# Kernel optimization log

Hardware: AMD Instinct MI355X
Metric: run time of the kernel (lower is better)

Reference implementation:

```python
import jax, jax.numpy as jnp
import numpy as np

NUM_HEADS = 16
BUDGET = 1024


def layer_norm(x, g, b, eps=1e-5):
    mu = jnp.mean(x, axis=-1, keepdims=True)
    var = jnp.mean((x - mu) ** 2, axis=-1, keepdims=True)
    return (x - mu) / jnp.sqrt(var + eps) * g + b


def setup_inputs() -> dict:
    key = jax.random.key(0)
    ks = jax.random.split(key, 6)
    B, N, D = 2, 2048, 1024
    H, Dh = NUM_HEADS, 1024 // NUM_HEADS
    sc = 1.0 / np.sqrt(D).astype(np.float32)
    X = jax.random.normal(ks[0], (B, N, D), jnp.float32)
    W_q = jax.random.normal(ks[1], (D, D), jnp.float32) * sc
    W_k = jax.random.normal(ks[2], (D, D), jnp.float32) * sc
    W_v = jax.random.normal(ks[3], (D, D), jnp.float32) * sc
    W_o = jax.random.normal(ks[4], (D, D), jnp.float32) * sc
    return dict(
        X=X, W_q=W_q, W_k=W_k, W_v=W_v, W_o=W_o,
        gamma_q=jnp.ones((D,), jnp.float32), beta_q=jnp.zeros((D,), jnp.float32),
        gamma_k=jnp.ones((D,), jnp.float32), beta_k=jnp.zeros((D,), jnp.float32),
        cache_k=jnp.zeros((B, H, BUDGET, Dh), jnp.float32),
        cache_v=jnp.zeros((B, H, BUDGET, Dh), jnp.float32),
        start_pos=0,
    )


def reference(X, W_q, W_k, W_v, W_o, gamma_q, beta_q, gamma_k, beta_k,
              cache_k, cache_v, start_pos):
    B, N, D = X.shape
    H = NUM_HEADS
    Dh = D // H
    budget = cache_k.shape[2]
    M = start_pos + N  # total kv length

    XQ = layer_norm(X @ W_q, gamma_q, beta_q).reshape(B, N, H, Dh).transpose(0, 2, 1, 3)
    XK = layer_norm(X @ W_k, gamma_k, beta_k).reshape(B, N, H, Dh).transpose(0, 2, 1, 3)
    XV = (X @ W_v).reshape(B, N, H, Dh).transpose(0, 2, 1, 3)

    K = jnp.concatenate([cache_k[:B, :, :start_pos], XK], axis=2)  # (B,H,M,Dh)
    V = jnp.concatenate([cache_v[:B, :, :start_pos], XV], axis=2)

    logits = jnp.einsum('bhnd,bhmd->bhnm', XQ, K) / np.float32(np.sqrt(Dh))
    n_idx = jnp.arange(N)[:, None]
    m_idx = jnp.arange(M)[None, :]
    causal_keep = (m_idx < start_pos) | ((m_idx - start_pos) <= n_idx)  # (N,M)
    logits = jnp.where(causal_keep, logits, -jnp.inf)

    # --- selection (eviction) scores from head 0 ---
    S = jax.nn.relu(logits[:, 0])                        # (B,N,M); relu(-inf)=0
    S = S.at[:, :, start_pos].set(0.0)                   # never evict <BOS>-like slot
    S = S.at[:, :, start_pos:].multiply(1.0 - jnp.eye(N, dtype=S.dtype))  # zero diagonal
    S = jnp.roll(S, 1, axis=1).at[:, 0, :].set(0.0)      # shift: scores apply from next query
    Fm = jnp.cumsum(S, axis=1)                           # (B,N,M) cumulative eviction scores

    # --- sequential heavy-hitter eviction ---
    unmasked0 = jnp.broadcast_to(jnp.arange(budget, dtype=jnp.int32), (B, budget))
    kpos = jnp.arange(budget, dtype=jnp.int32)[None, :]

    def step(unmasked, i):
        new_idx = jnp.concatenate(
            [unmasked, jnp.full((B, 1), i, unmasked.dtype)], axis=1)     # (B,budget+1)
        row = jax.lax.dynamic_index_in_dim(Fm, i - start_pos, axis=1, keepdims=False)  # (B,M)
        scores = jnp.take_along_axis(row, new_idx, axis=1)
        idx = jnp.argmax(scores, axis=-1)                                # (B,)
        evicted = jnp.take_along_axis(new_idx, idx[:, None], axis=1)[:, 0]
        unmasked = jnp.where(kpos < idx[:, None], new_idx[:, :budget], new_idx[:, 1:])
        return unmasked, evicted

    steps = jnp.arange(max(budget, start_pos), M, dtype=jnp.int32)       # (T,)
    _, evicts = jax.lax.scan(step, unmasked0, steps)                     # evicts (T,B)

    big = jnp.int32(M + start_pos + 1)
    evict_time = jnp.full((B, M), big, jnp.int32)
    evict_time = evict_time.at[jnp.arange(B, dtype=jnp.int32)[None, :], evicts].min(steps[:, None])
    # query row j is pruned from key m iff (j + start_pos) >= evict_time[m]
    prune_keep = (jnp.arange(N)[:, None] + start_pos) < evict_time[:, None, :]  # (B,N,M)

    logits = jnp.where(prune_keep[:, None], logits, -jnp.inf)
    attn = jax.nn.softmax(logits, axis=-1)
    O = jnp.einsum('bhnm,bhmd->bhnd', attn, V).transpose(0, 2, 1, 3).reshape(B, N, D)
    return O @ W_o
```

## Files before the change

### kernel.cpp

```cpp
#include <hip/hip_runtime.h>

#define B_    2
#define N_    2048
#define D_    1024
#define H_    16
#define DH_   64
#define M_    2048
#define ROWS_ 4096
#define BUD_  1024

typedef unsigned short u16;
typedef unsigned int   u32;
typedef unsigned long long u64;
typedef __attribute__((ext_vector_type(8))) short short8;
typedef __attribute__((ext_vector_type(4))) float floatx4;

__device__ __forceinline__ u16 f2b(float f) {
    u32 u = __float_as_uint(f);
    return (u16)((u + 0x7FFFu + ((u >> 16) & 1u)) >> 16);
}
__device__ __forceinline__ float b2f(u16 h) {
    return __uint_as_float(((u32)h) << 16);
}

__global__ __launch_bounds__(256) void cast_x_kernel(
    const float* __restrict__ X, u16* __restrict__ Xhi, u16* __restrict__ Xlo)
{
    int idx = (blockIdx.x * 256 + threadIdx.x) * 4;
    float4 v = *(const float4*)&X[idx];
    u16 h0 = f2b(v.x), h1 = f2b(v.y), h2 = f2b(v.z), h3 = f2b(v.w);
    ushort4 hv; hv.x = h0; hv.y = h1; hv.z = h2; hv.w = h3;
    *(ushort4*)&Xhi[idx] = hv;
    ushort4 lv;
    lv.x = f2b(v.x - b2f(h0)); lv.y = f2b(v.y - b2f(h1));
    lv.z = f2b(v.z - b2f(h2)); lv.w = f2b(v.w - b2f(h3));
    *(ushort4*)&Xlo[idx] = lv;
}

__global__ __launch_bounds__(1024) void cast_w_kernel(
    const float* __restrict__ W, u16* __restrict__ Whi, u16* __restrict__ Wlo,
    int do_lo)
{
    __shared__ float tile[32][33];
    int tx = threadIdx.x, ty = threadIdx.y;
    int x = blockIdx.x * 32 + tx, y = blockIdx.y * 32 + ty;
    tile[ty][tx] = W[(size_t)y * D_ + x];
    __syncthreads();
    float v = tile[tx][ty];
    int n = blockIdx.x * 32 + ty, k = blockIdx.y * 32 + tx;
    u16 h = f2b(v);
    Whi[(size_t)n * D_ + k] = h;
    if (do_lo) Wlo[(size_t)n * D_ + k] = f2b(v - b2f(h));
}

template<int MODE>
__device__ void gemm_core(
    const u16* __restrict__ Ah, const u16* __restrict__ Al,
    const u16* __restrict__ Bh, const u16* __restrict__ Bl,
    float* __restrict__ C, int bx, int m0)
{
    __shared__ __align__(16) u16 sAh[128 * 32];
    __shared__ __align__(16) u16 sBh[128 * 32];
    __shared__ __align__(16) u16 sAl[MODE ? 128 * 32 : 8];
    __shared__ __align__(16) u16 sBl[MODE ? 128 * 32 : 8];
    int tid = threadIdx.x;
    int lane = tid & 63, wv = tid >> 6;
    int wr = wv >> 1, wc = wv & 1;
    int quad = lane >> 4, l16 = lane & 15;
    int n0 = bx * 128;

    floatx4 acc[4][4];
    floatx4 zero = {0.f, 0.f, 0.f, 0.f};
#pragma unroll
    for (int i = 0; i < 4; ++i)
#pragma unroll
        for (int j = 0; j < 4; ++j) acc[i][j] = zero;

    for (int k0 = 0; k0 < 1024; k0 += 32) {
#pragma unroll
        for (int it = 0; it < 2; ++it) {
            int e = (tid + it * 256) * 8;
            int r = e >> 5, c = e & 31;
            *(uint4*)&sAh[e] = *(const uint4*)&Ah[(size_t)(m0 + r) * 1024 + k0 + c];
            *(uint4*)&sBh[e] = *(const uint4*)&Bh[(size_t)(n0 + r) * 1024 + k0 + c];
            if (MODE) {
                *(uint4*)&sAl[e] = *(const uint4*)&Al[(size_t)(m0 + r) * 1024 + k0 + c];
                *(uint4*)&sBl[e] = *(const uint4*)&Bl[(size_t)(n0 + r) * 1024 + k0 + c];
            }
        }
        __syncthreads();
        short8 ah[4], al[4], bh[4], bl[4];
#pragma unroll
        for (int x = 0; x < 4; ++x) {
            int ra = (wr * 64 + x * 16 + l16) * 32 + quad * 8;
            int rb = (wc * 64 + x * 16 + l16) * 32 + quad * 8;
            ah[x] = *(const short8*)&sAh[ra];
            bh[x] = *(const short8*)&sBh[rb];
            if (MODE) {
                al[x] = *(const short8*)&sAl[ra];
                bl[x] = *(const short8*)&sBl[rb];
            }
        }
#pragma unroll
        for (int mi = 0; mi < 4; ++mi)
#pragma unroll
            for (int ni = 0; ni < 4; ++ni) {
                acc[mi][ni] = __builtin_amdgcn_mfma_f32_16x16x32_bf16(
                    ah[mi], bh[ni], acc[mi][ni], 0, 0, 0);
                if (MODE) {
                    acc[mi][ni] = __builtin_amdgcn_mfma_f32_16x16x32_bf16(
                        ah[mi], bl[ni], acc[mi][ni], 0, 0, 0);
                    acc[mi][ni] = __builtin_amdgcn_mfma_f32_16x16x32_bf16(
                        al[mi], bh[ni], acc[mi][ni], 0, 0, 0);
                }
            }
        __syncthreads();
    }
#pragma unroll
    for (int mi = 0; mi < 4; ++mi)
#pragma unroll
        for (int ni = 0; ni < 4; ++ni)
#pragma unroll
            for (int r = 0; r < 4; ++r) {
                int row = m0 + wr * 64 + mi * 16 + quad * 4 + r;
                int col = n0 + wc * 64 + ni * 16 + l16;
                C[(size_t)row * 1024 + col] = acc[mi][ni][r];
            }
}

__global__ __launch_bounds__(256) void gemm_qkv_kernel(
    const u16* __restrict__ Xhi, const u16* __restrict__ Xlo,
    const u16* __restrict__ Wqh, const u16* __restrict__ Wql,
    const u16* __restrict__ Wkh, const u16* __restrict__ Wkl,
    const u16* __restrict__ Wvh,
    float* __restrict__ Yq, float* __restrict__ Yk, float* __restrict__ Yv)
{
    int m0 = blockIdx.y * 128;
    if (blockIdx.z == 0)
        gemm_core<1>(Xhi, Xlo, Wqh, Wql, Yq, blockIdx.x, m0);
    else if (blockIdx.z == 1)
        gemm_core<1>(Xhi, Xlo, Wkh, Wkl, Yk, blockIdx.x, m0);
    else
        gemm_core<0>(Xhi, nullptr, Wvh, nullptr, Yv, blockIdx.x, m0);
}

template<int MODE>
__global__ __launch_bounds__(256) void gemm_kernel_t(
    const u16* __restrict__ Ah, const u16* __restrict__ Al,
    const u16* __restrict__ Bh, const u16* __restrict__ Bl,
    float* __restrict__ C, int ymode)
{
    int by = blockIdx.y;
    int yidx = (ymode == 0) ? by : ((by < 8) ? by + 8 : by + 16);
    gemm_core<MODE>(Ah, Al, Bh, Bl, C, blockIdx.x, yidx * 128);
}

__global__ __launch_bounds__(256) void lnpack_all_kernel(
    const float* __restrict__ Yq, const float* __restrict__ Yk,
    const float* __restrict__ Yv,
    const float* __restrict__ gq, const float* __restrict__ bq,
    const float* __restrict__ gk, const float* __restrict__ bk,
    u16* __restrict__ Qb, u16* __restrict__ Kb, u16* __restrict__ Vb,
    float* __restrict__ q0s, float* __restrict__ k0s)
{
    const float* Y; const float* gamma; const float* beta;
    u16* Pk; float* head0; int do_ln;
    if (blockIdx.y == 0) { Y = Yq; gamma = gq; beta = bq; Pk = Qb; head0 = q0s; do_ln = 1; }
    else if (blockIdx.y == 1) { Y = Yk; gamma = gk; beta = bk; Pk = Kb; head0 = k0s; do_ln = 1; }
    else { Y = Yv; gamma = nullptr; beta = nullptr; Pk = Vb; head0 = nullptr; do_ln = 0; }

    int r = blockIdx.x;
    int tid = threadIdx.x;
    float4 v = *(const float4*)&Y[(size_t)r * D_ + tid * 4];
    float mu = 0.f, rsig = 1.f;
    __shared__ float sS[4], sQ[4];
    if (do_ln) {
        float s = v.x + v.y + v.z + v.w;
        float q = v.x * v.x + v.y * v.y + v.z * v.z + v.w * v.w;
#pragma unroll
        for (int d = 1; d < 64; d <<= 1) { s += __shfl_xor(s, d); q += __shfl_xor(q, d); }
        if ((tid & 63) == 0) { sS[tid >> 6] = s; sQ[tid >> 6] = q; }
        __syncthreads();
        s = sS[0] + sS[1] + sS[2] + sS[3];
        q = sQ[0] + sQ[1] + sQ[2] + sQ[3];
        mu = s * (1.f / 1024.f);
        float var = q * (1.f / 1024.f) - mu * mu;
        rsig = rsqrtf(var + 1e-5f);
    }
    int b = r >> 11, n = r & 2047;
    float xs[4] = {v.x, v.y, v.z, v.w};
#pragma unroll
    for (int j = 0; j < 4; ++j) {
        int c = tid * 4 + j;
        float val = do_ln ? ((xs[j] - mu) * rsig * gamma[c] + beta[c]) : xs[j];
        int h = c >> 6, dh = c & 63;
        Pk[(((size_t)b * H_ + h) * N_ + n) * DH_ + dh] = f2b(val);
        if (head0 && c < 64) head0[(size_t)r * 64 + c] = val;
    }
}

__global__ __launch_bounds__(256) void s64_kernel(
    const float* __restrict__ q0, const float* __restrict__ k0,
    float* __restrict__ S)
{
    int b = blockIdx.z;
    int n0 = blockIdx.y * 64, m0 = blockIdx.x * 64;
    int tid = threadIdx.x;
    int tx = tid & 15, ty = tid >> 4;
    floatx4 zero = {0.f, 0.f, 0.f, 0.f};
    if (m0 > n0 + 63) {
#pragma unroll
        for (int i = 0; i < 4; ++i) {
            int n = n0 + 4 * ty + i;
            *(floatx4*)&S[((size_t)b * N_ + n) * M_ + m0 + 4 * tx] = zero;
        }
        return;
    }
    __shared__ float sq[64][65], sk[64][65];
    {
        int r = tid >> 2, cseg = (tid & 3) * 16;
        const float* qrow = &q0[((size_t)b * N_ + n0 + r) * 64 + cseg];
        const float* krow = &k0[((size_t)b * N_ + m0 + r) * 64 + cseg];
#pragma unroll
        for (int u = 0; u < 4; ++u) {
            float4 qa = *(const float4*)&qrow[u * 4];
            sq[r][cseg + u * 4 + 0] = qa.x; sq[r][cseg + u * 4 + 1] = qa.y;
            sq[r][cseg + u * 4 + 2] = qa.z; sq[r][cseg + u * 4 + 3] = qa.w;
            float4 ka = *(const float4*)&krow[u * 4];
            sk[r][cseg + u * 4 + 0] = ka.x; sk[r][cseg + u * 4 + 1] = ka.y;
            sk[r][cseg + u * 4 + 2] = ka.z; sk[r][cseg + u * 4 + 3] = ka.w;
        }
    }
    __syncthreads();
    float acc[4][4];
#pragma unroll
    for (int i = 0; i < 4; ++i)
#pragma unroll
        for (int j = 0; j < 4; ++j) acc[i][j] = 0.f;
#pragma unroll 8
    for (int d = 0; d < 64; ++d) {
        float qv[4], kv[4];
#pragma unroll
        for (int i = 0; i < 4; ++i) qv[i] = sq[4 * ty + i][d];
#pragma unroll
        for (int j = 0; j < 4; ++j) kv[j] = sk[4 * tx + j][d];
#pragma unroll
        for (int i = 0; i < 4; ++i)
#pragma unroll
            for (int j = 0; j < 4; ++j) acc[i][j] += qv[i] * kv[j];
    }
#pragma unroll
    for (int i = 0; i < 4; ++i) {
        int n = n0 + 4 * ty + i;
        floatx4 out;
#pragma unroll
        for (int j = 0; j < 4; ++j) {
            int m = m0 + 4 * tx + j;
            out[j] = (m < n && m != 0) ? fmaxf(acc[i][j] * 0.125f, 0.f) : 0.f;
        }
        *(floatx4*)&S[((size_t)b * N_ + n) * M_ + m0 + 4 * tx] = out;
    }
}

__global__ __launch_bounds__(256) void p_kernel(const float* __restrict__ S,
                                                float* __restrict__ P)
{
    int b = blockIdx.z, c = blockIdx.y;
    int m = blockIdx.x * 256 + threadIdx.x;
    const float* base = S + ((size_t)b * N_ + c * 128) * M_ + m;
    float s = 0.f;
    for (int j = 0; j < 128; ++j) s += base[(size_t)j * M_];
    P[((size_t)b * 8 + c) * M_ + m] = s;
}

__device__ __forceinline__ void vsel(float& va, u32& la, float vb, u32 lb) {
    bool tk = vb > va;
    va = tk ? vb : va;
    la = tk ? lb : la;
}

template<int CTRL, int RMASK>
__device__ __forceinline__ void dpp_max_pack(float& v, u32& lo) {
    int hi = __float_as_int(v);
    int hi_o = __builtin_amdgcn_update_dpp(hi, hi, CTRL, RMASK, 0xF, false);
    int lo_o = __builtin_amdgcn_update_dpp((int)lo, (int)lo, CTRL, RMASK, 0xF, false);
    long long a = (long long)((((u64)(u32)hi) << 32) | lo);
    long long b = (long long)((((u64)(u32)hi_o) << 32) | (u32)lo_o);
    bool tk = b > a;
    v = tk ? __int_as_float(hi_o) : v;
    lo = tk ? (u32)lo_o : lo;
}

__device__ __forceinline__ void wave_argmax_to63(float& v, u32& lo) {
    dpp_max_pack<0x121, 0xF>(v, lo);
    dpp_max_pack<0x122, 0xF>(v, lo);
    dpp_max_pack<0x124, 0xF>(v, lo);
    dpp_max_pack<0x128, 0xF>(v, lo);
    dpp_max_pack<0x142, 0xA>(v, lo);
    dpp_max_pack<0x143, 0xC>(v, lo);
}

#define GLOAD(dst, voff, ptr, imm)                                    \
    asm volatile("global_load_dwordx4 %0, %1, %2 offset:" #imm        \
                 : "=v"(dst) : "v"(voff), "s"(ptr) : "memory")

#define ISSUE2(bank, row)                                             \
    {                                                                 \
        u32 r_ = (u32)((row) < 2047 ? (row) : 2047);                  \
        u32 vo = wbyte + r_ * 8192u;                                  \
        GLOAD(bank[0], vo, Sb, 0);                                    \
        GLOAD(bank[1], vo, Sb, 1024);                                 \
    }

#define VWAIT6()                                                      \
    do { asm volatile("s_waitcnt vmcnt(6)" ::: "memory");             \
         __builtin_amdgcn_sched_barrier(0); } while (0)
#define VWAIT0()                                                      \
    do { asm volatile("s_waitcnt vmcnt(0)" ::: "memory");             \
         __builtin_amdgcn_sched_barrier(0); } while (0)

__device__ __forceinline__ void evict_step4(
    int i, int t, int w, int par,
    const u32 (&lov)[2][4], float (&cum)[2][4], int (&evti)[2][4],
    const floatx4 (&bank)[2], uint2 (*spair)[4])
{
    const float NEGINF = __uint_as_float(0xFF800000u);
    float v0 = cum[0][0]; u32 l0 = lov[0][0];
    vsel(v0, l0, cum[0][1], lov[0][1]);
    float v1 = cum[0][2]; u32 l1 = lov[0][2];
    vsel(v1, l1, cum[0][3], lov[0][3]);
    vsel(v0, l0, v1, l1);
    float v2 = cum[1][0]; u32 l2 = lov[1][0];
    vsel(v2, l2, cum[1][1], lov[1][1]);
    float v3 = cum[1][2]; u32 l3 = lov[1][2];
    vsel(v3, l3, cum[1][3], lov[1][3]);
    vsel(v2, l2, v3, l3);
    vsel(v0, l0, v2, l2);
    wave_argmax_to63(v0, l0);
    if (t == 63) spair[par][w] = make_uint2(l0, (u32)__float_as_int(v0));
    asm volatile("s_waitcnt lgkmcnt(0)" ::: "memory");
    __builtin_amdgcn_sched_barrier(0);
    __builtin_amdgcn_s_barrier();
    __builtin_amdgcn_sched_barrier(0);
    uint2 q0 = spair[par][0], q1 = spair[par][1];
    uint2 q2 = spair[par][2], q3 = spair[par][3];
    long long k0 = (long long)((((u64)q0.y) << 32) | q0.x);
    long long k1 = (long long)((((u64)q1.y) << 32) | q1.x);
    long long k2 = (long long)((((u64)q2.y) << 32) | q2.x);
    long long k3 = (long long)((((u64)q3.y) << 32) | q3.x);
    long long ba = k0 > k1 ? k0 : k1;
    long long bb = k2 > k3 ? k2 : k3;
    long long bst = ba > bb ? ba : bb;
    const u32 lostar = (u32)(bst & 0xFFFFFFFFll);
#pragma unroll
    for (int c = 0; c < 2; ++c) {
        cum[c][0] += bank[c][0]; cum[c][1] += bank[c][1];
        cum[c][2] += bank[c][2]; cum[c][3] += bank[c][3];
    }
#pragma unroll
    for (int c = 0; c < 2; ++c)
#pragma unroll
        for (int e = 0; e < 4; ++e) {
            bool hit = (lov[c][e] == lostar);
            cum[c][e] = hit ? NEGINF : cum[c][e];
            evti[c][e] = hit ? i : evti[c][e];
        }
}

__device__ void evict_role(const float* __restrict__ S,
                           const float* __restrict__ P,
                           int* __restrict__ evt)
{
    int b = blockIdx.x;
    int tid = threadIdx.x;
    int w = tid >> 6, t = tid & 63;
    const float* Sb = S + (size_t)b * N_ * M_;
    int* evtb = evt + b * M_;
    const int mbase = 512 * w + 4 * t;
    const u32 wbyte = (u32)(2048 * w + 16 * t);
    __shared__ uint2 spair[2][4];
    u32 lov[2][4];
    int evti[2][4];
#pragma unroll
    for (int c = 0; c < 2; ++c)
#pragma unroll
        for (int e = 0; e < 4; ++e) {
            lov[c][e] = (u32)(2048 - (mbase + 256 * c + e));
            evti[c][e] = 0x3FFFFFFF;
        }
    float cum[2][4];
#pragma unroll
    for (int c = 0; c < 2; ++c) {
        float ax = 0.f, ay = 0.f, az = 0.f, aw = 0.f;
#pragma unroll
        for (int cc = 0; cc < 8; ++cc) {
            floatx4 pv = *(const floatx4*)&P[((size_t)b * 8 + cc) * M_ + mbase + 256 * c];
            ax += pv[0]; ay += pv[1]; az += pv[2]; aw += pv[3];
        }
        cum[c][0] = ax; cum[c][1] = ay; cum[c][2] = az; cum[c][3] = aw;
    }
    VWAIT0();
    floatx4 bA[2], bB[2], bC[2], bD[2];
    ISSUE2(bA, 1024)
    ISSUE2(bB, 1025)
    ISSUE2(bC, 1026)
    ISSUE2(bD, 1027)
#pragma unroll 1
    for (int ip = 1024; ip < 2048; ip += 4) {
        VWAIT6();
        evict_step4(ip + 0, t, w, 0, lov, cum, evti, bA, spair);
        ISSUE2(bA, ip + 4)
        VWAIT6();
        evict_step4(ip + 1, t, w, 1, lov, cum, evti, bB, spair);
        ISSUE2(bB, ip + 5)
        VWAIT6();
        evict_step4(ip + 2, t, w, 0, lov, cum, evti, bC, spair);
        ISSUE2(bC, ip + 6)
        VWAIT6();
        evict_step4(ip + 3, t, w, 1, lov, cum, evti, bD, spair);
        ISSUE2(bD, ip + 7)
    }
    VWAIT0();
#pragma unroll
    for (int c = 0; c < 2; ++c) {
        int4 o; o.x = evti[c][0]; o.y = evti[c][1];
        o.z = evti[c][2]; o.w = evti[c][3];
        *(int4*)&evtb[mbase + 256 * c] = o;
    }
}

__device__ void flash_role(
    const u16* __restrict__ Qb, const u16* __restrict__ Kb,
    const u16* __restrict__ Vb, const int* __restrict__ evtg,
    u16* __restrict__ Ob, int bh, int q0, int ktiles)
{
    int b = bh >> 4, h = bh & 15;
    int tid = threadIdx.x, lane = tid & 63, w = tid >> 6;
    int quad = lane >> 4, l16 = lane & 15;
    const u16* Qh = Qb + (size_t)bh * N_ * DH_;
    const u16* Kh = Kb + (size_t)bh * N_ * DH_;
    const u16* Vh = Vb + (size_t)bh * N_ * DH_;
    __shared__ __align__(16) u16 sK[64 * 64];
    __shared__ __align__(16) u16 sV[64 * 64];
    __shared__ __align__(16) u16 sP[4][16 * 64];
    __shared__ int sevt[64];

    short8 aq0 = *(const short8*)&Qh[(size_t)(q0 + w * 16 + l16) * 64 + quad * 8];
    short8 aq1 = *(const short8*)&Qh[(size_t)(q0 + w * 16 + l16) * 64 + quad * 8 + 32];

    floatx4 zero = {0.f, 0.f, 0.f, 0.f};
    floatx4 accO[4];
#pragma unroll
    for (int d = 0; d < 4; ++d) accO[d] = zero;
    float m_i[4] = {-1e30f, -1e30f, -1e30f, -1e30f};
    float l_i[4] = {0.f, 0.f, 0.f, 0.f};

    for (int kt = 0; kt < ktiles; ++kt) {
        int k0 = kt * 64;
#pragma unroll
        for (int it = 0; it < 2; ++it) {
            int e = (tid + it * 256) * 8;
            int r = e >> 6, c = e & 63;
            *(uint4*)&sK[e] = *(const uint4*)&Kh[(size_t)(k0 + r) * 64 + c];
            uint4 vv = *(const uint4*)&Vh[(size_t)(k0 + r) * 64 + c];
            sV[(c + 0) * 64 + r] = (u16)(vv.x & 0xFFFF);
            sV[(c + 1) * 64 + r] = (u16)(vv.x >> 16);
            sV[(c + 2) * 64 + r] = (u16)(vv.y & 0xFFFF);
            sV[(c + 3) * 64 + r] = (u16)(vv.y >> 16);
            sV[(c + 4) * 64 + r] = (u16)(vv.z & 0xFFFF);
            sV[(c + 5) * 64 + r] = (u16)(vv.z >> 16);
            sV[(c + 6) * 64 + r] = (u16)(vv.w & 0xFFFF);
            sV[(c + 7) * 64 + r] = (u16)(vv.w >> 16);
        }
        if (evtg && tid < 64) sevt[tid] = evtg[b * M_ + k0 + tid];
        __syncthreads();

        floatx4 lg[4];
        int nbase = q0 + w * 16 + quad * 4;
#pragma unroll
        for (int s = 0; s < 4; ++s) {
            floatx4 sc = zero;
            short8 bk0 = *(const short8*)&sK[(s * 16 + l16) * 64 + quad * 8];
            short8 bk1 = *(const short8*)&sK[(s * 16 + l16) * 64 + quad * 8 + 32];
            sc = __builtin_amdgcn_mfma_f32_16x16x32_bf16(aq0, bk0, sc, 0, 0, 0);
            sc = __builtin_amdgcn_mfma_f32_16x16x32_bf16(aq1, bk1, sc, 0, 0, 0);
            int m = k0 + s * 16 + l16;
            int ev = evtg ? sevt[s * 16 + l16] : 0x7FFFFFFF;
#pragma unroll
            for (int r = 0; r < 4; ++r) {
                int n = nbase + r;
                bool keep = (m <= n) && (n < ev);
                lg[s][r] = keep ? sc[r] * 0.125f : -1e30f;
            }
        }
        float mnew[4], scale[4], rs[4];
#pragma unroll
        for (int r = 0; r < 4; ++r) {
            float mx = fmaxf(fmaxf(lg[0][r], lg[1][r]), fmaxf(lg[2][r], lg[3][r]));
#pragma unroll
            for (int d = 1; d < 16; d <<= 1) mx = fmaxf(mx, __shfl_xor(mx, d));
            mnew[r] = fmaxf(m_i[r], mx);
            scale[r] = __expf(m_i[r] - mnew[r]);
            m_i[r] = mnew[r];
            rs[r] = 0.f;
        }
#pragma unroll
        for (int s = 0; s < 4; ++s)
#pragma unroll
            for (int r = 0; r < 4; ++r) {
                float p = __expf(lg[s][r] - mnew[r]);
                rs[r] += p;
                sP[w][(quad * 4 + r) * 64 + s * 16 + l16] = f2b(p);
            }
#pragma unroll
        for (int r = 0; r < 4; ++r) {
            float t_ = rs[r];
#pragma unroll
            for (int d = 1; d < 16; d <<= 1) t_ += __shfl_xor(t_, d);
            l_i[r] = l_i[r] * scale[r] + t_;
        }
#pragma unroll
        for (int dd = 0; dd < 4; ++dd) {
            accO[dd][0] *= scale[0]; accO[dd][1] *= scale[1];
            accO[dd][2] *= scale[2]; accO[dd][3] *= scale[3];
        }
        short8 ap0 = *(const short8*)&sP[w][l16 * 64 + quad * 8];
        short8 ap1 = *(const short8*)&sP[w][l16 * 64 + quad * 8 + 32];
#pragma unroll
        for (int dd = 0; dd < 4; ++dd) {
            short8 bv0 = *(const short8*)&sV[(dd * 16 + l16) * 64 + quad * 8];
            short8 bv1 = *(const short8*)&sV[(dd * 16 + l16) * 64 + quad * 8 + 32];
            accO[dd] = __builtin_amdgcn_mfma_f32_16x16x32_bf16(ap0, bv0, accO[dd], 0, 0, 0);
            accO[dd] = __builtin_amdgcn_mfma_f32_16x16x32_bf16(ap1, bv1, accO[dd], 0, 0, 0);
        }
        __syncthreads();
    }
#pragma unroll
    for (int dd = 0; dd < 4; ++dd)
#pragma unroll
        for (int r = 0; r < 4; ++r) {
            int n = q0 + w * 16 + quad * 4 + r;
            int col = h * 64 + dd * 16 + l16;
            Ob[((size_t)b * N_ + n) * D_ + col] = f2b(accO[dd][r] / l_i[r]);
        }
}

__global__ __launch_bounds__(256) void fused_evict_flash1(
    const float* __restrict__ S, const float* __restrict__ P,
    int* __restrict__ evt,
    const u16* __restrict__ Qb, const u16* __restrict__ Kb,
    const u16* __restrict__ Vb, u16* __restrict__ Ob)
{
    if (blockIdx.x < 2) {
        evict_role(S, P, evt);
    } else {
        int fid = blockIdx.x - 2;
        int bh = fid >> 4, j = fid & 15;
        flash_role(Qb, Kb, Vb, nullptr, Ob, bh, j * 64, j + 1);
    }
}

__global__ __launch_bounds__(256) void fused_flash2_gemmo1(
    const u16* __restrict__ Qb, const u16* __restrict__ Kb,
    const u16* __restrict__ Vb, const int* __restrict__ evt,
    u16* __restrict__ Ob, const u16* __restrict__ Woh,
    float* __restrict__ Out)
{
    if (blockIdx.x < 512) {
        int fid = blockIdx.x;
        int bh = fid >> 4, j = (fid & 15) + 16;
        flash_role(Qb, Kb, Vb, evt, Ob, bh, j * 64, j + 1);
    } else {
        int gid = blockIdx.x - 512;
        int bx = gid & 7, gy = gid >> 3;
        int yidx = (gy < 8) ? gy : gy + 8;
        gemm_core<0>((const u16*)Ob, nullptr, Woh, nullptr, Out, bx, yidx * 128);
    }
}

extern "C" void kernel_launch(void* const* d_in, const int* in_sizes, int n_in,
                              void* d_out, int out_size, void* d_ws, size_t ws_size,
                              hipStream_t stream)
{
    (void)in_sizes; (void)n_in; (void)out_size; (void)ws_size;
    const float* X  = (const float*)d_in[0];
    const float* Wq = (const float*)d_in[1];
    const float* Wk = (const float*)d_in[2];
    const float* Wv = (const float*)d_in[3];
    const float* Wo = (const float*)d_in[4];
    const float* gq = (const float*)d_in[5];
    const float* bq = (const float*)d_in[6];
    const float* gk = (const float*)d_in[7];
    const float* bk = (const float*)d_in[8];

    char* p = (char*)d_ws;
    const size_t SZ_XH = (size_t)ROWS_ * D_ * 2;
    const size_t SZ_W  = (size_t)D_ * D_ * 2;
    const size_t SZ_Y  = (size_t)ROWS_ * D_ * 4;
    const size_t SZ_PK = (size_t)ROWS_ * D_ * 2;
    const size_t SZ_H0 = (size_t)ROWS_ * 64 * 4;

    size_t o = 0;
    u16* Xhi = (u16*)(p + o); o += SZ_XH;
    u16* Xlo = (u16*)(p + o); o += SZ_XH;
    u16* Wqh = (u16*)(p + o); o += SZ_W;
    u16* Wql = (u16*)(p + o); o += SZ_W;
    u16* Wkh = (u16*)(p + o); o += SZ_W;
    u16* Wkl = (u16*)(p + o); o += SZ_W;
    u16* Wvh = (u16*)(p + o); o += SZ_W;
    u16* Woh = (u16*)(p + o); o += SZ_W;
    float* Yq = (float*)(p + o); size_t oYq = o; o += SZ_Y;
    float* Yk = (float*)(p + o); o += SZ_Y;
    float* Yv = (float*)(p + o); o += SZ_Y;
    u16* Qb = (u16*)(p + o); o += SZ_PK;
    u16* Kb = (u16*)(p + o); o += SZ_PK;
    u16* Vb = (u16*)(p + o); o += SZ_PK;
    float* q0s = (float*)(p + o); o += SZ_H0;
    float* k0s = (float*)(p + o); o += SZ_H0;
    float* Pp  = (float*)(p + o); o += (size_t)B_ * 8 * M_ * 4;
    int* evt   = (int*)(p + o);  o += (size_t)B_ * M_ * 4;
    float* S = (float*)(p + oYq);
    u16* Ob  = Xhi;

    cast_x_kernel<<<ROWS_ * D_ / (256 * 4), 256, 0, stream>>>(X, Xhi, Xlo);
    dim3 wgrid(32, 32), wblk(32, 32);
    cast_w_kernel<<<wgrid, wblk, 0, stream>>>(Wq, Wqh, Wql, 1);
    cast_w_kernel<<<wgrid, wblk, 0, stream>>>(Wk, Wkh, Wkl, 1);
    cast_w_kernel<<<wgrid, wblk, 0, stream>>>(Wv, Wvh, nullptr, 0);
    cast_w_kernel<<<wgrid, wblk, 0, stream>>>(Wo, Woh, nullptr, 0);

    gemm_qkv_kernel<<<dim3(8, 32, 3), 256, 0, stream>>>(
        Xhi, Xlo, Wqh, Wql, Wkh, Wkl, Wvh, Yq, Yk, Yv);

    lnpack_all_kernel<<<dim3(ROWS_, 3), 256, 0, stream>>>(
        Yq, Yk, Yv, gq, bq, gk, bk, Qb, Kb, Vb, q0s, k0s);

    s64_kernel<<<dim3(M_ / 64, N_ / 64, B_), 256, 0, stream>>>(q0s, k0s, S);
    p_kernel<<<dim3(M_ / 256, 8, B_), 256, 0, stream>>>(S, Pp);

    fused_evict_flash1<<<514, 256, 0, stream>>>(S, Pp, evt, Qb, Kb, Vb, Ob);
    fused_flash2_gemmo1<<<640, 256, 0, stream>>>(
        Qb, Kb, Vb, evt, Ob, Woh, (float*)d_out);
    gemm_kernel_t<0><<<dim3(8, 16), 256, 0, stream>>>(
        (const u16*)Ob, nullptr, Woh, nullptr, (float*)d_out, 2);
}
```

Baseline: 766.0 us.

## Resolve two serial eviction steps per block barrier using top-2 reduction

The serial eviction scan now handles two time steps per workgroup barrier. Step i's argmax is computed as before. For step i+1, each wave computes a best and second-best candidate with a DPP top-2 reduction over the updated cumulative scores, and after the barrier the second winner is taken as the best candidate other than the first winner. This halves the number of s_barrier and LDS round trips in the 1024-step serial loop, at the cost of more VALU work per step (64-bit packed compares and a top-2 reduction) and a changed load-wait depth.

```diff
diff --git a/kernel.cpp b/kernel.cpp
--- a/kernel.cpp
+++ b/kernel.cpp
@@ -273,31 +273,40 @@
     P[((size_t)b * 8 + c) * M_ + m] = s;
 }
 
-__device__ __forceinline__ void vsel(float& va, u32& la, float vb, u32 lb) {
-    bool tk = vb > va;
-    va = tk ? vb : va;
-    la = tk ? lb : la;
-}
-
+__device__ __forceinline__ long long maxll(long long a, long long b) {
+    return a > b ? a : b;
+}
+__device__ __forceinline__ long long mkpack(float v, u32 lo) {
+    return (long long)((((u64)(u32)__float_as_int(v)) << 32) | (u64)lo);
+}
 template<int CTRL, int RMASK>
-__device__ __forceinline__ void dpp_max_pack(float& v, u32& lo) {
-    int hi = __float_as_int(v);
-    int hi_o = __builtin_amdgcn_update_dpp(hi, hi, CTRL, RMASK, 0xF, false);
-    int lo_o = __builtin_amdgcn_update_dpp((int)lo, (int)lo, CTRL, RMASK, 0xF, false);
-    long long a = (long long)((((u64)(u32)hi) << 32) | lo);
-    long long b = (long long)((((u64)(u32)hi_o) << 32) | (u32)lo_o);
-    bool tk = b > a;
-    v = tk ? __int_as_float(hi_o) : v;
-    lo = tk ? (u32)lo_o : lo;
-}
-
-__device__ __forceinline__ void wave_argmax_to63(float& v, u32& lo) {
-    dpp_max_pack<0x121, 0xF>(v, lo);
-    dpp_max_pack<0x122, 0xF>(v, lo);
-    dpp_max_pack<0x124, 0xF>(v, lo);
-    dpp_max_pack<0x128, 0xF>(v, lo);
-    dpp_max_pack<0x142, 0xA>(v, lo);
-    dpp_max_pack<0x143, 0xC>(v, lo);
+__device__ __forceinline__ long long dpp_ll(long long p) {
+    int hi = (int)((u64)p >> 32), lo = (int)(u32)(u64)p;
+    int ho = __builtin_amdgcn_update_dpp(hi, hi, CTRL, RMASK, 0xF, false);
+    int lo2 = __builtin_amdgcn_update_dpp(lo, lo, CTRL, RMASK, 0xF, false);
+    return (long long)((((u64)(u32)ho) << 32) | (u32)lo2);
+}
+template<int CTRL, int RMASK>
+__device__ __forceinline__ void dpp_t1(long long& B) {
+    B = maxll(B, dpp_ll<CTRL, RMASK>(B));
+}
+template<int CTRL, int RMASK>
+__device__ __forceinline__ void dpp_t2(long long& B, long long& S) {
+    long long Bo = dpp_ll<CTRL, RMASK>(B);
+    long long So = dpp_ll<CTRL, RMASK>(S);
+    bool gt = Bo > B;
+    long long nS = gt ? maxll(B, So) : maxll(S, Bo);
+    B = gt ? Bo : B;
+    S = nS;
+}
+__device__ __forceinline__ long long wave_t1_63(long long B) {
+    dpp_t1<0x121, 0xF>(B); dpp_t1<0x122, 0xF>(B); dpp_t1<0x124, 0xF>(B);
+    dpp_t1<0x128, 0xF>(B); dpp_t1<0x142, 0xA>(B); dpp_t1<0x143, 0xC>(B);
+    return B;
+}
+__device__ __forceinline__ void wave_t2_63(long long& B, long long& S) {
+    dpp_t2<0x121, 0xF>(B, S); dpp_t2<0x122, 0xF>(B, S); dpp_t2<0x124, 0xF>(B, S);
+    dpp_t2<0x128, 0xF>(B, S); dpp_t2<0x142, 0xA>(B, S); dpp_t2<0x143, 0xC>(B, S);
 }
 
 #define GLOAD(dst, voff, ptr, imm)                                    \
@@ -312,59 +321,86 @@
         GLOAD(bank[1], vo, Sb, 1024);                                 \
     }
 
-#define VWAIT6()                                                      \
-    do { asm volatile("s_waitcnt vmcnt(6)" ::: "memory");             \
+#define VWAIT4()                                                      \
+    do { asm volatile("s_waitcnt vmcnt(4)" ::: "memory");             \
          __builtin_amdgcn_sched_barrier(0); } while (0)
 #define VWAIT0()                                                      \
     do { asm volatile("s_waitcnt vmcnt(0)" ::: "memory");             \
          __builtin_amdgcn_sched_barrier(0); } while (0)
 
-__device__ __forceinline__ void evict_step4(
+__device__ __forceinline__ long long pk2(uint2 q) {
+    return (long long)((((u64)q.y) << 32) | q.x);
+}
+
+__device__ __forceinline__ void evict_pair(
     int i, int t, int w, int par,
     const u32 (&lov)[2][4], float (&cum)[2][4], int (&evti)[2][4],
-    const floatx4 (&bank)[2], uint2 (*spair)[4])
+    const floatx4 (&bi)[2], const floatx4 (&bi1)[2],
+    uint2 (*spair)[4][3])
 {
     const float NEGINF = __uint_as_float(0xFF800000u);
-    float v0 = cum[0][0]; u32 l0 = lov[0][0];
-    vsel(v0, l0, cum[0][1], lov[0][1]);
-    float v1 = cum[0][2]; u32 l1 = lov[0][2];
-    vsel(v1, l1, cum[0][3], lov[0][3]);
-    vsel(v0, l0, v1, l1);
-    float v2 = cum[1][0]; u32 l2 = lov[1][0];
-    vsel(v2, l2, cum[1][1], lov[1][1]);
-    float v3 = cum[1][2]; u32 l3 = lov[1][2];
-    vsel(v3, l3, cum[1][3], lov[1][3]);
-    vsel(v2, l2, v3, l3);
-    vsel(v0, l0, v2, l2);
-    wave_argmax_to63(v0, l0);
-    if (t == 63) spair[par][w] = make_uint2(l0, (u32)__float_as_int(v0));
+    long long a = mkpack(cum[0][0], lov[0][0]);
+    a = maxll(a, mkpack(cum[0][1], lov[0][1]));
+    a = maxll(a, mkpack(cum[0][2], lov[0][2]));
+    a = maxll(a, mkpack(cum[0][3], lov[0][3]));
+    a = maxll(a, mkpack(cum[1][0], lov[1][0]));
+    a = maxll(a, mkpack(cum[1][1], lov[1][1]));
+    a = maxll(a, mkpack(cum[1][2], lov[1][2]));
+    a = maxll(a, mkpack(cum[1][3], lov[1][3]));
+    a = wave_t1_63(a);
+#pragma unroll
+    for (int c = 0; c < 2; ++c) {
+        cum[c][0] += bi[c][0]; cum[c][1] += bi[c][1];
+        cum[c][2] += bi[c][2]; cum[c][3] += bi[c][3];
+    }
+    long long Bst = mkpack(cum[0][0], lov[0][0]);
+    long long Snd = (long long)0x8000000000000000ULL;
+#define INS_(cc, ee)                                                   \
+    { long long q_ = mkpack(cum[cc][ee], lov[cc][ee]);                 \
+      bool gt_ = q_ > Bst;                                             \
+      Snd = gt_ ? Bst : maxll(Snd, q_);                                \
+      Bst = gt_ ? q_ : Bst; }
+    INS_(0, 1) INS_(0, 2) INS_(0, 3)
+    INS_(1, 0) INS_(1, 1) INS_(1, 2) INS_(1, 3)
+#undef INS_
+    wave_t2_63(Bst, Snd);
+    if (t == 63) {
+        spair[par][w][0] = make_uint2((u32)(u64)a,   (u32)((u64)a >> 32));
+        spair[par][w][1] = make_uint2((u32)(u64)Bst, (u32)((u64)Bst >> 32));
+        spair[par][w][2] = make_uint2((u32)(u64)Snd, (u32)((u64)Snd >> 32));
+    }
     asm volatile("s_waitcnt lgkmcnt(0)" ::: "memory");
     __builtin_amdgcn_sched_barrier(0);
     __builtin_amdgcn_s_barrier();
     __builtin_amdgcn_sched_barrier(0);
-    uint2 q0 = spair[par][0], q1 = spair[par][1];
-    uint2 q2 = spair[par][2], q3 = spair[par][3];
-    long long k0 = (long long)((((u64)q0.y) << 32) | q0.x);
-    long long k1 = (long long)((((u64)q1.y) << 32) | q1.x);
-    long long k2 = (long long)((((u64)q2.y) << 32) | q2.x);
-    long long k3 = (long long)((((u64)q3.y) << 32) | q3.x);
-    long long ba = k0 > k1 ? k0 : k1;
-    long long bb = k2 > k3 ? k2 : k3;
-    long long bst = ba > bb ? ba : bb;
-    const u32 lostar = (u32)(bst & 0xFFFFFFFFll);
+    long long A0 = pk2(spair[par][0][0]), A1 = pk2(spair[par][1][0]);
+    long long A2 = pk2(spair[par][2][0]), A3 = pk2(spair[par][3][0]);
+    long long B0 = pk2(spair[par][0][1]), B1 = pk2(spair[par][1][1]);
+    long long B2 = pk2(spair[par][2][1]), B3 = pk2(spair[par][3][1]);
+    long long S0 = pk2(spair[par][0][2]), S1 = pk2(spair[par][1][2]);
+    long long S2 = pk2(spair[par][2][2]), S3 = pk2(spair[par][3][2]);
+    const long long w1 = maxll(maxll(A0, A1), maxll(A2, A3));
+    const u32 w1lo = (u32)(u64)w1;
+    long long C0 = ((u32)(u64)B0 == w1lo) ? S0 : B0;
+    long long C1 = ((u32)(u64)B1 == w1lo) ? S1 : B1;
+    long long C2 = ((u32)(u64)B2 == w1lo) ? S2 : B2;
+    long long C3 = ((u32)(u64)B3 == w1lo) ? S3 : B3;
+    const long long w2 = maxll(maxll(C0, C1), maxll(C2, C3));
+    const u32 w2lo = (u32)(u64)w2;
+#pragma unroll
+    for (int c = 0; c < 2; ++c)
+#pragma unroll
+        for (int e = 0; e < 4; ++e) {
+            bool h1 = (lov[c][e] == w1lo);
+            bool h2 = (lov[c][e] == w2lo);
+            cum[c][e] = (h1 || h2) ? NEGINF : cum[c][e];
+            evti[c][e] = h1 ? i : (h2 ? (i + 1) : evti[c][e]);
+        }
 #pragma unroll
     for (int c = 0; c < 2; ++c) {
-        cum[c][0] += bank[c][0]; cum[c][1] += bank[c][1];
-        cum[c][2] += bank[c][2]; cum[c][3] += bank[c][3];
-    }
-#pragma unroll
-    for (int c = 0; c < 2; ++c)
-#pragma unroll
-        for (int e = 0; e < 4; ++e) {
-            bool hit = (lov[c][e] == lostar);
-            cum[c][e] = hit ? NEGINF : cum[c][e];
-            evti[c][e] = hit ? i : evti[c][e];
-        }
+        cum[c][0] += bi1[c][0]; cum[c][1] += bi1[c][1];
+        cum[c][2] += bi1[c][2]; cum[c][3] += bi1[c][3];
+    }
 }
 
 __device__ void evict_role(const float* __restrict__ S,
@@ -378,7 +414,7 @@
     int* evtb = evt + b * M_;
     const int mbase = 512 * w + 4 * t;
     const u32 wbyte = (u32)(2048 * w + 16 * t);
-    __shared__ uint2 spair[2][4];
+    __shared__ uint2 spair[2][4][3];
     u32 lov[2][4];
     int evti[2][4];
 #pragma unroll
@@ -407,17 +443,13 @@
     ISSUE2(bD, 1027)
 #pragma unroll 1
     for (int ip = 1024; ip < 2048; ip += 4) {
-        VWAIT6();
-        evict_step4(ip + 0, t, w, 0, lov, cum, evti, bA, spair);
+        VWAIT4();
+        evict_pair(ip + 0, t, w, 0, lov, cum, evti, bA, bB, spair);
         ISSUE2(bA, ip + 4)
-        VWAIT6();
-        evict_step4(ip + 1, t, w, 1, lov, cum, evti, bB, spair);
         ISSUE2(bB, ip + 5)
-        VWAIT6();
-        evict_step4(ip + 2, t, w, 0, lov, cum, evti, bC, spair);
+        VWAIT4();
+        evict_pair(ip + 2, t, w, 1, lov, cum, evti, bC, bD, spair);
         ISSUE2(bC, ip + 6)
-        VWAIT6();
-        evict_step4(ip + 3, t, w, 1, lov, cum, evti, bD, spair);
         ISSUE2(bD, ip + 7)
     }
     VWAIT0();
```

Result: slower. 893.8 us (+16.7%).
